# Optimization experiments

Hardware: AMD Instinct MI355X
Metric: run time of the kernel (lower is better)

The kernel has to match this reference:

```python
import jax, jax.numpy as jnp
import numpy as np

N_NODES = 50000
N_EDGES = 800000
SD = 128
N_GRAPHS = 128
HL = 4
VOCAB = 1340
N_CLASSES = 41
BN_EPS = 1e-5


def setup_inputs() -> dict:
    key = jax.random.key(0)
    ks = jax.random.split(key, 20)
    s = 1.0 / np.sqrt(SD)
    inp = {
        "node_ids": jax.random.randint(ks[0], (N_NODES,), 0, VOCAB),
        "edge_index": jax.random.randint(ks[1], (2, N_EDGES), 0, N_NODES),
        "batch": jnp.sort(jax.random.randint(ks[2], (N_NODES,), 0, N_GRAPHS)),
        "emb": jax.random.normal(ks[3], (VOCAB, SD)) * 0.05,
        "in_W1": jax.random.normal(ks[4], (SD, SD)) * s,
        "in_b1": jnp.zeros((SD,)),
        "in_W2": jax.random.normal(ks[5], (SD, SD)) * s,
        "in_b2": jnp.zeros((SD,)),
        "bn_gamma": jnp.ones((SD,)),
        "bn_beta": jnp.zeros((SD,)),
        "bn_mean": jnp.zeros((SD,)),
        "bn_var": jnp.ones((SD,)),
        "out_W1": jax.random.normal(ks[6], (SD, SD)) * s,
        "out_b1": jnp.zeros((SD,)),
        "out_W2": jax.random.normal(ks[7], (SD, SD)) * s,
        "out_b2": jnp.zeros((SD,)),
        "fc1_W": jax.random.normal(ks[8], (SD, SD)) * s,
        "fc1_b": jnp.zeros((SD,)),
        "fc2_W": jax.random.normal(ks[9], (N_CLASSES, SD)) * s,
        "fc2_b": jnp.zeros((N_CLASSES,)),
    }
    return inp


def reference(node_ids, edge_index, batch, emb, in_W1, in_b1, in_W2, in_b2,
              bn_gamma, bn_beta, bn_mean, bn_var,
              out_W1, out_b1, out_W2, out_b2, fc1_W, fc1_b, fc2_W, fc2_b):
    src, dst = edge_index[0], edge_index[1]

    def gin(x, W1, b1, W2, b2):
        # GINConv with eps=0: mlp(x + sum_{j in N(i)} x_j)
        agg = jax.ops.segment_sum(x[src], dst, num_segments=N_NODES)
        h = x + agg
        h = jnp.maximum(h @ W1.T + b1, 0.0)
        return h @ W2.T + b2

    def bn(x):
        # eval-mode BatchNorm1d with running stats
        return (x - bn_mean) * (bn_gamma / jnp.sqrt(bn_var + BN_EPS)) + bn_beta

    x = emb[node_ids]  # [N, SD]
    x = bn(jnp.maximum(gin(x, in_W1, in_b1, in_W2, in_b2), 0.0))
    for _ in range(HL):  # shared weights, repeated hl times
        x = bn(jnp.maximum(gin(x, in_W1, in_b1, in_W2, in_b2), 0.0))
    x = jnp.maximum(gin(x, out_W1, out_b1, out_W2, out_b2), 0.0)
    pooled = jax.ops.segment_sum(x, batch, num_segments=N_GRAPHS)  # [G, SD]
    h = jnp.maximum(pooled @ fc1_W.T + fc1_b, 0.0)
    return h @ fc2_W.T + fc2_b  # [G, 41]
```

## Files before the change

kernel.cpp:

```cpp
#include <hip/hip_runtime.h>

#define NN 50000
#define NE 800000
#define NG 128
#define NC 41
#define CAP 64

typedef __attribute__((ext_vector_type(8))) short bfrag8;
typedef __attribute__((ext_vector_type(4))) float facc4;

__device__ __forceinline__ float bf2f(unsigned short u) {
  union { unsigned int i; float f; } v; v.i = ((unsigned int)u) << 16; return v.f;
}
__device__ __forceinline__ unsigned short f2bf(float f) {
  union { float f; unsigned int i; } v; v.f = f;
  unsigned int x = v.i;
  x += 0x7fffu + ((x >> 16) & 1u);
  return (unsigned short)(x >> 16);
}
__device__ __forceinline__ void acc_u4(const uint4 u, float* a) {
  union { unsigned int i; float f; } c;
  c.i = u.x << 16;          a[0] += c.f;
  c.i = u.x & 0xffff0000u;  a[1] += c.f;
  c.i = u.y << 16;          a[2] += c.f;
  c.i = u.y & 0xffff0000u;  a[3] += c.f;
  c.i = u.z << 16;          a[4] += c.f;
  c.i = u.z & 0xffff0000u;  a[5] += c.f;
  c.i = u.w << 16;          a[6] += c.f;
  c.i = u.w & 0xffff0000u;  a[7] += c.f;
}
__device__ __forceinline__ unsigned int pack2(float lo, float hi) {
  return (unsigned int)f2bf(lo) | ((unsigned int)f2bf(hi) << 16);
}

__global__ void prep_kernel(const float* __restrict__ W1, const float* __restrict__ W2,
                            const float* __restrict__ oW1, const float* __restrict__ oW2,
                            const float* __restrict__ gamma, const float* __restrict__ beta,
                            const float* __restrict__ mean, const float* __restrict__ var,
                            unsigned short* W1b, unsigned short* W2b,
                            unsigned short* oW1b, unsigned short* oW2b,
                            float* scale, float* shift) {
  int i = blockIdx.x * 256 + threadIdx.x;
  if (i < 128 * 128) {
    W1b[i] = f2bf(W1[i]);
    W2b[i] = f2bf(W2[i]);
    oW1b[i] = f2bf(oW1[i]);
    oW2b[i] = f2bf(oW2[i]);
  }
  if (i < 128) {
    float s = gamma[i] * rsqrtf(var[i] + 1e-5f);
    scale[i] = s;
    shift[i] = beta[i] - mean[i] * s;
  }
}

__global__ void embed_kernel(const int* __restrict__ node_ids, const float* __restrict__ emb,
                             unsigned short* __restrict__ xb) {
  int idx = blockIdx.x * 256 + threadIdx.x;
  if (idx >= NN * 32) return;
  int node = idx >> 5, f = (idx & 31) * 4;
  const float4 v = *(const float4*)&emb[node_ids[node] * 128 + f];
  ushort4 o;
  o.x = f2bf(v.x); o.y = f2bf(v.y); o.z = f2bf(v.z); o.w = f2bf(v.w);
  *(ushort4*)&xb[node * 128 + f] = o;
}

__global__ void fill_kernel(const int* __restrict__ ei, int* __restrict__ cnt,
                            int* __restrict__ srclist) {
  int e = blockIdx.x * 256 + threadIdx.x;
  if (e >= NE) return;
  int s = ei[e];
  int d = ei[NE + e];
  int pos = atomicAdd(&cnt[d], 1);
  if (pos < CAP) srclist[d * CAP + pos] = s;
}

__global__ __launch_bounds__(256) void agg_kernel(const unsigned short* __restrict__ xb,
                                                  const int* __restrict__ cnt,
                                                  const int* __restrict__ srclist,
                                                  unsigned short* __restrict__ hb) {
  int tid = threadIdx.x;
  int wave = tid >> 6;
  int lane = tid & 63;
  int node = blockIdx.x * 4 + wave;
  if (node >= NN) return;
  int slot = lane >> 4;
  int chunk = lane & 15;
  int f = chunk * 8;

  float a[8];
#pragma unroll
  for (int i = 0; i < 8; ++i) a[i] = 0.f;
  if (slot == 0) acc_u4(*(const uint4*)&xb[node * 128 + f], a);

  int deg = cnt[node];
  if (deg > CAP) deg = CAP;
  const int* lst = &srclist[node * CAP];

  int j = slot;
  for (; j + 12 < deg; j += 16) {
    int n0 = lst[j];
    int n1 = lst[j + 4];
    int n2 = lst[j + 8];
    int n3 = lst[j + 12];
    uint4 u0 = *(const uint4*)&xb[n0 * 128 + f];
    uint4 u1 = *(const uint4*)&xb[n1 * 128 + f];
    uint4 u2 = *(const uint4*)&xb[n2 * 128 + f];
    uint4 u3 = *(const uint4*)&xb[n3 * 128 + f];
    acc_u4(u0, a); acc_u4(u1, a); acc_u4(u2, a); acc_u4(u3, a);
  }
  for (; j + 4 < deg; j += 8) {
    int n0 = lst[j];
    int n1 = lst[j + 4];
    uint4 u0 = *(const uint4*)&xb[n0 * 128 + f];
    uint4 u1 = *(const uint4*)&xb[n1 * 128 + f];
    acc_u4(u0, a); acc_u4(u1, a);
  }
  if (j < deg) {
    uint4 u = *(const uint4*)&xb[lst[j] * 128 + f];
    acc_u4(u, a);
  }

#pragma unroll
  for (int i = 0; i < 8; ++i) {
    a[i] += __shfl_xor(a[i], 16, 64);
    a[i] += __shfl_xor(a[i], 32, 64);
  }
  if (slot == 0) {
    uint4 o;
    o.x = pack2(a[0], a[1]); o.y = pack2(a[2], a[3]);
    o.z = pack2(a[4], a[5]); o.w = pack2(a[6], a[7]);
    *(uint4*)&hb[node * 128 + f] = o;
  }
}

__global__ __launch_bounds__(256) void mlp_kernel(const unsigned short* __restrict__ A,
                                                  const unsigned short* __restrict__ W1b,
                                                  const unsigned short* __restrict__ W2b,
                                                  const float* __restrict__ bias1,
                                                  const float* __restrict__ bias2,
                                                  const float* __restrict__ scale,
                                                  const float* __restrict__ shift,
                                                  unsigned short* __restrict__ Out,
                                                  int M, int mode) {
  __shared__ unsigned short sW1[128 * 128];
  __shared__ unsigned short sW2[128 * 128];
  __shared__ unsigned short sA[64 * 128];
  int tid = threadIdx.x;
  int bRow = blockIdx.x * 64;

  const uint4* gw1 = (const uint4*)W1b;
  const uint4* gw2 = (const uint4*)W2b;
#pragma unroll
  for (int p = 0; p < 8; ++p) {
    int g = p * 256 + tid;
    int r = g >> 4, b = g & 15;
    int ph = (b + r) & 15;
    *(uint4*)&sW1[(r * 16 + ph) * 8] = gw1[g];
    *(uint4*)&sW2[(r * 16 + ph) * 8] = gw2[g];
  }
#pragma unroll
  for (int p = 0; p < 4; ++p) {
    int g = p * 256 + tid;
    int r = g >> 4, b = g & 15;
    int ph = (b + r) & 15;
    int grow = bRow + r;
    uint4 v = {0u, 0u, 0u, 0u};
    if (grow < M) v = *(const uint4*)&A[grow * 128 + b * 8];
    *(uint4*)&sA[(r * 16 + ph) * 8] = v;
  }
  __syncthreads();

  int wave = tid >> 6;
  int lane = tid & 63;
  int l16 = lane & 15;
  int quad = lane >> 4;
  int arow = wave * 16 + l16;

  {
    bfrag8 af[4];
#pragma unroll
    for (int k = 0; k < 4; ++k) {
      int ph = (k * 4 + quad + arow) & 15;
      af[k] = *(const bfrag8*)&sA[(arow * 16 + ph) * 8];
    }
    facc4 acc[8];
#pragma unroll
    for (int t = 0; t < 8; ++t) acc[t] = (facc4){0.f, 0.f, 0.f, 0.f};
#pragma unroll
    for (int k = 0; k < 4; ++k) {
#pragma unroll
      for (int t = 0; t < 8; ++t) {
        int r = t * 16 + l16;
        int ph = (k * 4 + quad + r) & 15;
        bfrag8 bf = *(const bfrag8*)&sW1[(r * 16 + ph) * 8];
        acc[t] = __builtin_amdgcn_mfma_f32_16x16x32_bf16(af[k], bf, acc[t], 0, 0, 0);
      }
    }
#pragma unroll
    for (int t = 0; t < 8; ++t) {
      int col = t * 16 + l16;
      float b = bias1[col];
      int cb = col >> 3, ce = col & 7;
#pragma unroll
      for (int i = 0; i < 4; ++i) {
        int row = wave * 16 + quad * 4 + i;
        float v = acc[t][i] + b;
        int ph = (cb + row) & 15;
        sA[(row * 16 + ph) * 8 + ce] = f2bf(v > 0.f ? v : 0.f);
      }
    }
  }

  {
    bfrag8 af[4];
#pragma unroll
    for (int k = 0; k < 4; ++k) {
      int ph = (k * 4 + quad + arow) & 15;
      af[k] = *(const bfrag8*)&sA[(arow * 16 + ph) * 8];
    }
    facc4 acc[8];
#pragma unroll
    for (int t = 0; t < 8; ++t) acc[t] = (facc4){0.f, 0.f, 0.f, 0.f};
#pragma unroll
    for (int k = 0; k < 4; ++k) {
#pragma unroll
      for (int t = 0; t < 8; ++t) {
        int r = t * 16 + l16;
        int ph = (k * 4 + quad + r) & 15;
        bfrag8 bf = *(const bfrag8*)&sW2[(r * 16 + ph) * 8];
        acc[t] = __builtin_amdgcn_mfma_f32_16x16x32_bf16(af[k], bf, acc[t], 0, 0, 0);
      }
    }
#pragma unroll
    for (int t = 0; t < 8; ++t) {
      int col = t * 16 + l16;
      float b = bias2[col];
      float sc = 1.f, sh = 0.f;
      if (mode == 1) { sc = scale[col]; sh = shift[col]; }
      int cb = col >> 3, ce = col & 7;
#pragma unroll
      for (int i = 0; i < 4; ++i) {
        int row = wave * 16 + quad * 4 + i;
        float v = acc[t][i] + b;
        v = v > 0.f ? v : 0.f;
        if (mode == 1) v = v * sc + sh;
        int ph = (cb + row) & 15;
        sA[(row * 16 + ph) * 8 + ce] = f2bf(v);
      }
    }
  }
  __syncthreads();

#pragma unroll
  for (int p = 0; p < 4; ++p) {
    int g = p * 256 + tid;
    int r = g >> 4, b = g & 15;
    int ph = (b + r) & 15;
    int grow = bRow + r;
    if (grow < M)
      *(uint4*)&Out[grow * 128 + b * 8] = *(const uint4*)&sA[(r * 16 + ph) * 8];
  }
}

__global__ __launch_bounds__(128) void pool_kernel(const unsigned short* __restrict__ xb,
                                                   const int* __restrict__ batch,
                                                   float* __restrict__ pooled) {
  const int CHUNK = 128;
  int start = blockIdx.x * CHUNK;
  int end = start + CHUNK;
  if (end > NN) end = NN;
  int f = threadIdx.x;
  float acc = 0.f;
  int cur = -1;
  for (int i = start; i < end; ++i) {
    int b = batch[i];
    if (b != cur) {
      if (cur >= 0) atomicAdd(&pooled[cur * 128 + f], acc);
      cur = b;
      acc = 0.f;
    }
    acc += bf2f(xb[i * 128 + f]);
  }
  if (cur >= 0) atomicAdd(&pooled[cur * 128 + f], acc);
}

__global__ void fc1_kernel(const float* __restrict__ pooled, const float* __restrict__ W,
                           const float* __restrict__ b, float* __restrict__ out) {
  int idx = blockIdx.x * 256 + threadIdx.x;
  if (idx >= NG * 128) return;
  int r = idx >> 7, c = idx & 127;
  float acc = 0.f;
  for (int k = 0; k < 128; ++k) acc += pooled[r * 128 + k] * W[c * 128 + k];
  acc += b[c];
  out[idx] = acc > 0.f ? acc : 0.f;
}

__global__ void fc2_kernel(const float* __restrict__ h1, const float* __restrict__ W,
                           const float* __restrict__ b, float* __restrict__ out) {
  int idx = blockIdx.x * 256 + threadIdx.x;
  if (idx >= NG * NC) return;
  int r = idx / NC, c = idx % NC;
  float acc = 0.f;
  for (int k = 0; k < 128; ++k) acc += h1[r * 128 + k] * W[c * 128 + k];
  out[idx] = acc + b[c];
}

extern "C" void kernel_launch(void* const* d_in, const int* in_sizes, int n_in,
                              void* d_out, int out_size, void* d_ws, size_t ws_size,
                              hipStream_t stream) {
  const int* node_ids = (const int*)d_in[0];
  const int* edge_index = (const int*)d_in[1];
  const int* batch = (const int*)d_in[2];
  const float* emb = (const float*)d_in[3];
  const float* in_W1 = (const float*)d_in[4];
  const float* in_b1 = (const float*)d_in[5];
  const float* in_W2 = (const float*)d_in[6];
  const float* in_b2 = (const float*)d_in[7];
  const float* bn_gamma = (const float*)d_in[8];
  const float* bn_beta = (const float*)d_in[9];
  const float* bn_mean = (const float*)d_in[10];
  const float* bn_var = (const float*)d_in[11];
  const float* out_W1 = (const float*)d_in[12];
  const float* out_b1 = (const float*)d_in[13];
  const float* out_W2 = (const float*)d_in[14];
  const float* out_b2 = (const float*)d_in[15];
  const float* fc1_W = (const float*)d_in[16];
  const float* fc1_b = (const float*)d_in[17];
  const float* fc2_W = (const float*)d_in[18];
  const float* fc2_b = (const float*)d_in[19];
  float* out = (float*)d_out;

  char* ws = (char*)d_ws;
  size_t off = 0;
  auto alloc = [&](size_t bytes) {
    char* p = ws + off;
    off = (off + bytes + 255) & ~(size_t)255;
    return p;
  };
  unsigned short* xb = (unsigned short*)alloc((size_t)NN * 128 * 2);
  unsigned short* hb = (unsigned short*)alloc((size_t)NN * 128 * 2);
  int* srclist = (int*)alloc((size_t)NN * CAP * 4);
  int* cnt = (int*)alloc((size_t)NN * 4);
  unsigned short* W1b = (unsigned short*)alloc(128 * 128 * 2);
  unsigned short* W2b = (unsigned short*)alloc(128 * 128 * 2);
  unsigned short* oW1b = (unsigned short*)alloc(128 * 128 * 2);
  unsigned short* oW2b = (unsigned short*)alloc(128 * 128 * 2);
  float* bnscale = (float*)alloc(128 * 4);
  float* bnshift = (float*)alloc(128 * 4);
  float* pooled = (float*)alloc(NG * 128 * 4);
  float* h1 = (float*)alloc(NG * 128 * 4);

  hipMemsetAsync(cnt, 0, (size_t)NN * 4, stream);
  hipMemsetAsync(pooled, 0, (size_t)NG * 128 * 4, stream);

  prep_kernel<<<64, 256, 0, stream>>>(in_W1, in_W2, out_W1, out_W2,
                                      bn_gamma, bn_beta, bn_mean, bn_var,
                                      W1b, W2b, oW1b, oW2b, bnscale, bnshift);
  fill_kernel<<<(NE + 255) / 256, 256, 0, stream>>>(edge_index, cnt, srclist);
  embed_kernel<<<(NN * 32 + 255) / 256, 256, 0, stream>>>(node_ids, emb, xb);

  int mlp_blocks = (NN + 63) / 64;
  for (int l = 0; l < 6; ++l) {
    const unsigned short* w1 = (l < 5) ? W1b : oW1b;
    const unsigned short* w2 = (l < 5) ? W2b : oW2b;
    const float* b1 = (l < 5) ? in_b1 : out_b1;
    const float* b2 = (l < 5) ? in_b2 : out_b2;
    int mode2 = (l < 5) ? 1 : 0;
    agg_kernel<<<(NN + 3) / 4, 256, 0, stream>>>(xb, cnt, srclist, hb);
    mlp_kernel<<<mlp_blocks, 256, 0, stream>>>(hb, w1, w2, b1, b2, bnscale, bnshift,
                                               xb, NN, mode2);
  }

  pool_kernel<<<(NN + 127) / 128, 128, 0, stream>>>(xb, batch, pooled);
  fc1_kernel<<<(NG * 128 + 255) / 256, 256, 0, stream>>>(pooled, fc1_W, fc1_b, h1);
  fc2_kernel<<<(NG * NC + 255) / 256, 256, 0, stream>>>(h1, fc2_W, fc2_b, out);
}
```

Before: 507.8 us.

## Fuse neighbor aggregation into MLP kernel with 256-row 1024-thread blocks

Merges the separate gather-sum kernel and the two-layer MLP kernel into a single per-layer kernel. Each 1024-thread block aggregates 256 rows straight into shared memory, then runs the MFMA MLP on them. Two buffers alternate between input and output across layers. This drops the intermediate global write and read of the aggregated features and halves the launch count. In exchange there are only about 196 blocks, fewer than the 256 CUs, and the 128KB of LDS per block limits each CU to one block, so the latency-bound gather may run at low occupancy.

```diff
diff --git a/kernel.cpp b/kernel.cpp
--- a/kernel.cpp
+++ b/kernel.cpp
@@ -75,104 +75,87 @@
   if (pos < CAP) srclist[d * CAP + pos] = s;
 }
 
-__global__ __launch_bounds__(256) void agg_kernel(const unsigned short* __restrict__ xb,
-                                                  const int* __restrict__ cnt,
-                                                  const int* __restrict__ srclist,
-                                                  unsigned short* __restrict__ hb) {
-  int tid = threadIdx.x;
-  int wave = tid >> 6;
-  int lane = tid & 63;
-  int node = blockIdx.x * 4 + wave;
-  if (node >= NN) return;
-  int slot = lane >> 4;
-  int chunk = lane & 15;
-  int f = chunk * 8;
-
-  float a[8];
-#pragma unroll
-  for (int i = 0; i < 8; ++i) a[i] = 0.f;
-  if (slot == 0) acc_u4(*(const uint4*)&xb[node * 128 + f], a);
-
-  int deg = cnt[node];
-  if (deg > CAP) deg = CAP;
-  const int* lst = &srclist[node * CAP];
-
-  int j = slot;
-  for (; j + 12 < deg; j += 16) {
-    int n0 = lst[j];
-    int n1 = lst[j + 4];
-    int n2 = lst[j + 8];
-    int n3 = lst[j + 12];
-    uint4 u0 = *(const uint4*)&xb[n0 * 128 + f];
-    uint4 u1 = *(const uint4*)&xb[n1 * 128 + f];
-    uint4 u2 = *(const uint4*)&xb[n2 * 128 + f];
-    uint4 u3 = *(const uint4*)&xb[n3 * 128 + f];
-    acc_u4(u0, a); acc_u4(u1, a); acc_u4(u2, a); acc_u4(u3, a);
-  }
-  for (; j + 4 < deg; j += 8) {
-    int n0 = lst[j];
-    int n1 = lst[j + 4];
-    uint4 u0 = *(const uint4*)&xb[n0 * 128 + f];
-    uint4 u1 = *(const uint4*)&xb[n1 * 128 + f];
-    acc_u4(u0, a); acc_u4(u1, a);
-  }
-  if (j < deg) {
-    uint4 u = *(const uint4*)&xb[lst[j] * 128 + f];
-    acc_u4(u, a);
-  }
-
-#pragma unroll
-  for (int i = 0; i < 8; ++i) {
-    a[i] += __shfl_xor(a[i], 16, 64);
-    a[i] += __shfl_xor(a[i], 32, 64);
-  }
-  if (slot == 0) {
-    uint4 o;
-    o.x = pack2(a[0], a[1]); o.y = pack2(a[2], a[3]);
-    o.z = pack2(a[4], a[5]); o.w = pack2(a[6], a[7]);
-    *(uint4*)&hb[node * 128 + f] = o;
-  }
-}
-
-__global__ __launch_bounds__(256) void mlp_kernel(const unsigned short* __restrict__ A,
-                                                  const unsigned short* __restrict__ W1b,
-                                                  const unsigned short* __restrict__ W2b,
-                                                  const float* __restrict__ bias1,
-                                                  const float* __restrict__ bias2,
-                                                  const float* __restrict__ scale,
-                                                  const float* __restrict__ shift,
-                                                  unsigned short* __restrict__ Out,
-                                                  int M, int mode) {
+__global__ __launch_bounds__(1024, 4) void layer_kernel(
+    const unsigned short* __restrict__ Xin,
+    const int* __restrict__ cnt,
+    const int* __restrict__ srclist,
+    const unsigned short* __restrict__ W1b,
+    const unsigned short* __restrict__ W2b,
+    const float* __restrict__ bias1,
+    const float* __restrict__ bias2,
+    const float* __restrict__ scale,
+    const float* __restrict__ shift,
+    unsigned short* __restrict__ Xout,
+    int mode) {
   __shared__ unsigned short sW1[128 * 128];
   __shared__ unsigned short sW2[128 * 128];
-  __shared__ unsigned short sA[64 * 128];
+  __shared__ unsigned short sA[256 * 128];
   int tid = threadIdx.x;
-  int bRow = blockIdx.x * 64;
+  int bRow = blockIdx.x * 256;
 
   const uint4* gw1 = (const uint4*)W1b;
   const uint4* gw2 = (const uint4*)W2b;
 #pragma unroll
-  for (int p = 0; p < 8; ++p) {
-    int g = p * 256 + tid;
+  for (int p = 0; p < 2; ++p) {
+    int g = p * 1024 + tid;
     int r = g >> 4, b = g & 15;
     int ph = (b + r) & 15;
     *(uint4*)&sW1[(r * 16 + ph) * 8] = gw1[g];
     *(uint4*)&sW2[(r * 16 + ph) * 8] = gw2[g];
   }
-#pragma unroll
-  for (int p = 0; p < 4; ++p) {
-    int g = p * 256 + tid;
-    int r = g >> 4, b = g & 15;
-    int ph = (b + r) & 15;
-    int grow = bRow + r;
-    uint4 v = {0u, 0u, 0u, 0u};
-    if (grow < M) v = *(const uint4*)&A[grow * 128 + b * 8];
-    *(uint4*)&sA[(r * 16 + ph) * 8] = v;
-  }
-  __syncthreads();
 
   int wave = tid >> 6;
   int lane = tid & 63;
+  int slot = lane >> 4;
+  int chunk = lane & 15;
+  int f = chunk * 8;
+
+  for (int i = 0; i < 16; ++i) {
+    int lrow = wave * 16 + i;
+    int grow = bRow + lrow;
+    float a[8];
+#pragma unroll
+    for (int q = 0; q < 8; ++q) a[q] = 0.f;
+    if (grow < NN) {
+      if (slot == 0) acc_u4(*(const uint4*)&Xin[grow * 128 + f], a);
+      int deg = cnt[grow];
+      if (deg > CAP) deg = CAP;
+      const int* lst = &srclist[grow * CAP];
+      int j = slot;
+      for (; j + 12 < deg; j += 16) {
+        int n0 = lst[j], n1 = lst[j + 4], n2 = lst[j + 8], n3 = lst[j + 12];
+        uint4 u0 = *(const uint4*)&Xin[n0 * 128 + f];
+        uint4 u1 = *(const uint4*)&Xin[n1 * 128 + f];
+        uint4 u2 = *(const uint4*)&Xin[n2 * 128 + f];
+        uint4 u3 = *(const uint4*)&Xin[n3 * 128 + f];
+        acc_u4(u0, a); acc_u4(u1, a); acc_u4(u2, a); acc_u4(u3, a);
+      }
+      for (; j + 4 < deg; j += 8) {
+        int n0 = lst[j], n1 = lst[j + 4];
+        uint4 u0 = *(const uint4*)&Xin[n0 * 128 + f];
+        uint4 u1 = *(const uint4*)&Xin[n1 * 128 + f];
+        acc_u4(u0, a); acc_u4(u1, a);
+      }
+      if (j < deg) {
+        uint4 u = *(const uint4*)&Xin[lst[j] * 128 + f];
+        acc_u4(u, a);
+      }
+    }
+#pragma unroll
+    for (int q = 0; q < 8; ++q) {
+      a[q] += __shfl_xor(a[q], 16, 64);
+      a[q] += __shfl_xor(a[q], 32, 64);
+    }
+    if (slot == 0) {
+      int ph = (chunk + lrow) & 15;
+      uint4 o;
+      o.x = pack2(a[0], a[1]); o.y = pack2(a[2], a[3]);
+      o.z = pack2(a[4], a[5]); o.w = pack2(a[6], a[7]);
+      *(uint4*)&sA[(lrow * 16 + ph) * 8] = o;
+    }
+  }
+  __syncthreads();
+
   int l16 = lane & 15;
   int quad = lane >> 4;
   int arow = wave * 16 + l16;
@@ -254,12 +237,12 @@
 
 #pragma unroll
   for (int p = 0; p < 4; ++p) {
-    int g = p * 256 + tid;
+    int g = p * 1024 + tid;
     int r = g >> 4, b = g & 15;
     int ph = (b + r) & 15;
     int grow = bRow + r;
-    if (grow < M)
-      *(uint4*)&Out[grow * 128 + b * 8] = *(const uint4*)&sA[(r * 16 + ph) * 8];
+    if (grow < NN)
+      *(uint4*)&Xout[grow * 128 + b * 8] = *(const uint4*)&sA[(r * 16 + ph) * 8];
   }
 }
 
@@ -360,16 +343,17 @@
   fill_kernel<<<(NE + 255) / 256, 256, 0, stream>>>(edge_index, cnt, srclist);
   embed_kernel<<<(NN * 32 + 255) / 256, 256, 0, stream>>>(node_ids, emb, xb);
 
-  int mlp_blocks = (NN + 63) / 64;
+  int blocks = (NN + 255) / 256;
+  unsigned short* bufs[2] = {xb, hb};
   for (int l = 0; l < 6; ++l) {
     const unsigned short* w1 = (l < 5) ? W1b : oW1b;
     const unsigned short* w2 = (l < 5) ? W2b : oW2b;
     const float* b1 = (l < 5) ? in_b1 : out_b1;
     const float* b2 = (l < 5) ? in_b2 : out_b2;
     int mode2 = (l < 5) ? 1 : 0;
-    agg_kernel<<<(NN + 3) / 4, 256, 0, stream>>>(xb, cnt, srclist, hb);
-    mlp_kernel<<<mlp_blocks, 256, 0, stream>>>(hb, w1, w2, b1, b2, bnscale, bnshift,
-                                               xb, NN, mode2);
+    layer_kernel<<<blocks, 1024, 0, stream>>>(bufs[l & 1], cnt, srclist, w1, w2,
+                                              b1, b2, bnscale, bnshift,
+                                              bufs[(l + 1) & 1], mode2);
   }
 
   pool_kernel<<<(NN + 127) / 128, 128, 0, stream>>>(xb, batch, pooled);
```

New measurement: 556.4 us. 1.1x slower.
